# Kernel tuning notes

Hardware: AMD Instinct MI355X
Metric: run time of the kernel (lower is better)

The kernel has to match this reference:

```python
import jax, jax.numpy as jnp
import numpy as np

B, L, D, H = 16, 1024, 128, 256


def setup_inputs() -> dict:
    key = jax.random.key(0)
    ks = jax.random.split(key, 32)
    inp = {
        "x": jax.random.normal(ks[0], (B, L, D), jnp.float32),
        "y": jax.random.normal(ks[1], (B, L, D), jnp.float32),
        "z": jax.random.normal(ks[2], (B, L, D), jnp.float32),
        "len_x": jax.random.randint(ks[3], (B,), L // 2, L + 1, dtype=jnp.int32),
        "len_y": jax.random.randint(ks[4], (B,), L // 2, L + 1, dtype=jnp.int32),
        "len_z": jax.random.randint(ks[5], (B,), L // 2, L + 1, dtype=jnp.int32),
    }
    s1 = (2.0 / (D + H)) ** 0.5  # xavier-normal for first layer
    s2 = (2.0 / (H + D)) ** 0.5
    i = 6
    for name in ("W1", "B1", "W2", "B2"):
        inp[f"{name}_l1_w"] = jax.random.normal(ks[i + 0], (D, H), jnp.float32) * s1
        inp[f"{name}_l1_b"] = jnp.zeros((H,), jnp.float32)
        inp[f"{name}_l2_w"] = jax.random.normal(ks[i + 1], (H, D), jnp.float32) * s2
        inp[f"{name}_l2_b"] = jnp.zeros((D,), jnp.float32)
        i += 2
    return inp


def _mlp(c, w1, b1, w2, b2):
    h = jax.nn.gelu(c @ w1 + b1, approximate=False)  # torch nn.GELU = exact erf form
    return h @ w2 + b2


def _batched_ragged_dft(xc, lengths, inverse):
    # Per-sample DFT over the first lengths[i] timesteps; rows/cols >= l are zero.
    _, Ls, _ = xc.shape
    t = jnp.arange(Ls, dtype=jnp.int32)
    kt = t[:, None] * t[None, :]                      # [L,L] integer k*t
    l = lengths[:, None, None]                        # [B,1,1]
    ktm = kt[None, :, :] % l                          # exact phase reduction mod l
    sign = 1.0 if inverse else -1.0
    phase = sign * 2.0 * jnp.pi * ktm.astype(jnp.float32) / l.astype(jnp.float32)
    mask = (t[None, :, None] < l) & (t[None, None, :] < l)
    E = jnp.where(mask, jnp.exp(1j * phase).astype(jnp.complex64), 0.0)
    if inverse:
        E = E / l.astype(jnp.complex64)
    return jnp.einsum("bkt,btd->bkd", E, xc)


def _complex_relu(f):
    # torch: where(|z|>0, |z|*exp(i*angle(z)), 0)
    mag = jnp.abs(f)
    safe = jnp.where(mag > 0, f, jnp.asarray(1.0 + 0.0j, jnp.complex64))
    act = jnp.abs(safe) * jnp.exp(1j * jnp.angle(safe))
    return jnp.where(mag > 0, act.astype(jnp.complex64), 0.0)


def reference(x, y, z, len_x, len_y, len_z,
              W1_l1_w, W1_l1_b, W1_l2_w, W1_l2_b,
              B1_l1_w, B1_l1_b, B1_l2_w, B1_l2_b,
              W2_l1_w, W2_l1_b, W2_l2_w, W2_l2_b,
              B2_l1_w, B2_l1_b, B2_l2_w, B2_l2_b):
    x_freq = _batched_ragged_dft(x.astype(jnp.complex64), len_x, inverse=False)
    c1 = jnp.sum(y, axis=1) / len_y[:, None].astype(jnp.float32)
    c2 = jnp.sum(z, axis=1) / len_z[:, None].astype(jnp.float32)
    W1 = _mlp(c1, W1_l1_w, W1_l1_b, W1_l2_w, W1_l2_b).astype(jnp.complex64)
    b1 = _mlp(c1, B1_l1_w, B1_l1_b, B1_l2_w, B1_l2_b).astype(jnp.complex64)
    W2 = _mlp(c2, W2_l1_w, W2_l1_b, W2_l2_w, W2_l2_b).astype(jnp.complex64)
    b2 = _mlp(c2, B2_l1_w, B2_l1_b, B2_l2_w, B2_l2_b).astype(jnp.complex64)
    filtered = x_freq * (1.0 + (W1 + W2)[:, None, :] / 2.0) + (b1 + b2)[:, None, :] / 2.0
    activated = _complex_relu(filtered)
    x_recon = _batched_ragged_dft(activated, len_x, inverse=True)
    return x_recon.real
```

## Files before the change

kernel.cpp:

```cpp
#include <hip/hip_runtime.h>
#include <math.h>

constexpr int NB = 16;
constexpr int SL = 1024;
constexpr int ND = 128;
constexpr int NH = 256;
constexpr int NSTILE = 18;
constexpr int NKTILE = 17;
constexpr int EPAD = 584;

constexpr size_t PLANE_S = (size_t)NB * 8 * NSTILE * 1024;
constexpr size_t PLANE_K = (size_t)NB * 8 * NKTILE * 1024;
constexpr size_t CS_OFF = 0;
constexpr size_t DD_OFF = PLANE_S;
constexpr size_t FR_OFF = 2 * PLANE_S;
constexpr size_t FI_OFF = 2 * PLANE_S + PLANE_K;
constexpr size_t F32B      = PLANE_S + PLANE_K;
constexpr size_t P_OFF     = F32B;
constexpr size_t SCALE_OFF = P_OFF + 2 * 16 * 16 * 128;
constexpr size_t BIAS_OFF  = SCALE_OFF + NB * ND;

typedef float          f32x4 __attribute__((ext_vector_type(4)));
typedef unsigned int   u32x4 __attribute__((ext_vector_type(4)));
typedef unsigned short u16x8 __attribute__((ext_vector_type(8)));

__device__ __forceinline__ unsigned short f2bf(float f) {
    unsigned u = __float_as_uint(f);
    return (unsigned short)((u + 0x7FFFu + ((u >> 16) & 1u)) >> 16);
}
__device__ __forceinline__ float hw_sin(float rev) {
    float r; asm("v_sin_f32 %0, %1" : "=v"(r) : "v"(rev)); return r;
}
__device__ __forceinline__ float hw_cos(float rev) {
    float r; asm("v_cos_f32 %0, %1" : "=v"(r) : "v"(rev)); return r;
}
__device__ __forceinline__ void mfma16(f32x4& acc, u32x4 a, u32x4 b) {
    asm("v_mfma_f32_16x16x32_bf16 %0, %1, %2, %0" : "+v"(acc) : "v"(a), "v"(b));
}
__device__ __forceinline__ float4 f4add(float4 a, float4 b) {
    return make_float4(a.x + b.x, a.y + b.y, a.z + b.z, a.w + b.w);
}

__global__ __launch_bounds__(256) void k_front(const float* __restrict__ x,
                                               const float* __restrict__ y,
                                               const float* __restrict__ z,
                                               const int* __restrict__ len_x,
                                               float* __restrict__ wsf,
                                               unsigned short* __restrict__ wsb,
                                               float* __restrict__ out) {
    const int blk = blockIdx.x;
    const int tid = threadIdx.x;
    __shared__ float4 red4[256];

    if (blk < 512) {
        const int ch  = blk & 15;
        const int b   = (blk >> 4) & 15;
        const int src = blk >> 8;
        const float* base = (src == 0 ? y : z) + ((size_t)b * SL + ch * 64) * ND;
        const int dg = tid & 31;
        const int tq = tid >> 5;
        float4 s = make_float4(0.f, 0.f, 0.f, 0.f);
#pragma unroll
        for (int j = 0; j < 8; ++j)
            s = f4add(s, *(const float4*)&base[(size_t)(tq + 8 * j) * ND + dg * 4]);
        red4[tid] = s;
        __syncthreads();
        if (tq < 4) red4[tid] = f4add(red4[tid], red4[tid + 128]);
        __syncthreads();
        if (tq < 2) red4[tid] = f4add(red4[tid], red4[tid + 64]);
        __syncthreads();
        if (tq == 0) {
            const float4 r = f4add(red4[dg], red4[dg + 32]);
            *(float4*)&wsf[P_OFF + ((size_t)((src * NB + b) * 16 + ch)) * ND + dg * 4] = r;
        }
        return;
    }

    if (blk < 800) {
        const int pb = blk - 512;
        const int bx = pb % NSTILE;
        const int b  = pb / NSTILE;
        const int l = len_x[b];
        const int NS = (l >> 1) + 1;
        const int d = tid & 127;
        const int slot = tid >> 7;
        const int dblk = d >> 4, dw = d & 15;
#pragma unroll
        for (int it = 0; it < 2; ++it) {
            const int sb = (bx * 4 + slot * 2 + it) * 8;
            u16x8 cb, db;
#pragma unroll
            for (int j = 0; j < 8; ++j) {
                const int s = sb + j;
                float c = 0.f, dd = 0.f;
                if (s < NS) {
                    const float a = x[((size_t)b * SL + s) * ND + d];
                    float p = 0.f;
                    if (s > 0 && 2 * s != l) p = x[((size_t)b * SL + (l - s)) * ND + d];
                    c = a + p; dd = a - p;
                }
                cb[j] = f2bf(c); db[j] = f2bf(dd);
            }
            const int sg = (sb >> 3) & 3;
            const size_t ro = ((size_t)((b * 8 + dblk) * NSTILE) + bx) * 1024 + sg * 128 + dw * 8;
            *(u16x8*)&wsb[CS_OFF + ro] = cb;
            *(u16x8*)&wsb[DD_OFF + ro] = db;
            if (sb + 7 >= NS && sb < NKTILE * 32) {
                const u16x8 zz = {0, 0, 0, 0, 0, 0, 0, 0};
                const size_t ko = ((size_t)((b * 8 + dblk) * NKTILE) + (sb >> 5)) * 1024 + sg * 128 + dw * 8;
                *(u16x8*)&wsb[FR_OFF + ko] = zz;
                *(u16x8*)&wsb[FI_OFF + ko] = zz;
            }
        }
        return;
    }

    {
        const int zb = blk - 800;
        const int b = zb >> 3;
        const int seg = zb & 7;
        const int l = len_x[b];
        const int row = 512 + seg * 64 + (tid >> 2);
        if (row >= l) {
            const int c16 = (tid & 3) * 32;
            float* p = &out[((size_t)b * SL + row) * ND + c16];
            const float4 zz = make_float4(0.f, 0.f, 0.f, 0.f);
#pragma unroll
            for (int q = 0; q < 8; ++q)
                *(float4*)&p[q * 4] = zz;
        }
        return;
    }
}

__global__ __launch_bounds__(512) void k_fwd_mlp(
    const int* __restrict__ len_x,
    const int* __restrict__ len_y, const int* __restrict__ len_z,
    float* __restrict__ wsf, unsigned short* __restrict__ wsb,
    const float* __restrict__ W1w1, const float* __restrict__ W1b1,
    const float* __restrict__ W1w2, const float* __restrict__ W1b2,
    const float* __restrict__ B1w1, const float* __restrict__ B1b1,
    const float* __restrict__ B1w2, const float* __restrict__ B1b2,
    const float* __restrict__ W2w1, const float* __restrict__ W2b1,
    const float* __restrict__ W2w2, const float* __restrict__ W2b2,
    const float* __restrict__ B2w1, const float* __restrict__ B2b1,
    const float* __restrict__ B2w2, const float* __restrict__ B2b2) {
    const int tid = threadIdx.x;

    if (blockIdx.x >= 528) {
        const int mb = blockIdx.x - 528;
        const int pair = mb & 1;
        const int b    = mb >> 1;

        const float* w1a = pair ? B1w1 : W1w1;  const float* b1a = pair ? B1b1 : W1b1;
        const float* w2a = pair ? B1w2 : W1w2;  const float* b2a = pair ? B1b2 : W1b2;
        const float* w1b = pair ? B2w1 : W2w1;  const float* b1b = pair ? B2b1 : W2b1;
        const float* w2b = pair ? B2w2 : W2w2;  const float* b2b = pair ? B2b2 : W2b2;

        __shared__ float c1s[ND], c2s[ND];
        __shared__ float h0[NH], h1[NH];
        __shared__ float oa[ND], ob[ND];

        if (tid < ND) {
            float s = 0.f;
            for (int ch = 0; ch < 16; ++ch)
                s += wsf[P_OFF + ((size_t)((0 * NB + b) * 16 + ch)) * ND + tid];
            c1s[tid] = s / (float)len_y[b];
        } else if (tid < 256) {
            const int d = tid - ND;
            float s = 0.f;
            for (int ch = 0; ch < 16; ++ch)
                s += wsf[P_OFF + ((size_t)((1 * NB + b) * 16 + ch)) * ND + d];
            c2s[d] = s / (float)len_z[b];
        }
        __syncthreads();

        if (tid < 256) {
            const int j = tid;
            float s0 = b1a[j], s1 = b1b[j];
            for (int i = 0; i < ND; ++i) {
                s0 = fmaf(c1s[i], w1a[i * NH + j], s0);
                s1 = fmaf(c2s[i], w1b[i * NH + j], s1);
            }
            h0[j] = 0.5f * s0 * (1.f + erff(s0 * 0.7071067811865475f));
            h1[j] = 0.5f * s1 * (1.f + erff(s1 * 0.7071067811865475f));
        }
        __syncthreads();

        if (tid < 256) {
            const bool second = tid >= ND;
            const int d = second ? tid - ND : tid;
            const float* w = second ? w2b : w2a;
            const float* hh = second ? h1 : h0;
            float s = second ? b2b[d] : b2a[d];
            for (int j = 0; j < NH; ++j)
                s = fmaf(hh[j], w[j * ND + d], s);
            if (second) ob[d] = s; else oa[d] = s;
        }
        __syncthreads();

        if (tid < ND) {
            if (pair == 0)
                wsf[SCALE_OFF + b * ND + tid] = 1.f + 0.5f * (oa[tid] + ob[tid]);
            else
                wsf[BIAS_OFF  + b * ND + tid] = 0.5f * (oa[tid] + ob[tid]);
        }
        return;
    }

    const int bid = blockIdx.x;
    const int b7 = bid & 7;
    const int q  = bid >> 3;
    const int b  = (q / 33) * 8 + b7;
    const int kbase = (q % 33) * 16;

    const int l = len_x[b];
    const int NS = (l >> 1) + 1;
    if (kbase >= NS) return;
    const float invl = 1.f / (float)l;
    const float fl = (float)l;

    __shared__ __align__(16) unsigned short Ec[16][EPAD];
    __shared__ __align__(16) unsigned short Es[16][EPAD];

    const int lane = tid & 63;
    const int wave8 = tid >> 6;
    const int shalf = wave8 >> 2;
    const int w4    = wave8 & 3;
    const int lrow = lane & 15, lkg = lane >> 4;

    if (tid < 256) {
        const int row = tid >> 4;
        const int colbase = (tid & 15) * 36;
        const int kk = kbase + row;
#pragma unroll 6
        for (int j = 0; j < 36; j += 2) {
            unsigned cw = 0, sw = 0;
#pragma unroll
            for (int h = 0; h < 2; ++h) {
                const int sg = colbase + j + h;
                float cv = 0.f, sv = 0.f;
                if (sg < NS) {
                    const float ks = (float)(kk * sg);
                    float idxf = fmaf(-fl, floorf(ks * invl), ks);
                    idxf = (idxf < 0.f) ? idxf + fl : idxf;
                    const float rev = idxf * invl;
                    cv = hw_cos(rev);
                    sv = -hw_sin(rev);
                }
                cw |= (unsigned)f2bf(cv) << (16 * h);
                sw |= (unsigned)f2bf(sv) << (16 * h);
            }
            *(unsigned*)&Ec[row][colbase + j] = cw;
            *(unsigned*)&Es[row][colbase + j] = sw;
        }
    }
    __syncthreads();

    f32x4 accR[2], accI[2];
#pragma unroll
    for (int t = 0; t < 2; ++t) { accR[t] = 0.f; accI[t] = 0.f; }

    const size_t tb0 = ((size_t)((b * 8 + 2 * w4 + 0) * NSTILE)) * 1024 + lane * 8;
    const size_t tb1 = ((size_t)((b * 8 + 2 * w4 + 1) * NSTILE)) * 1024 + lane * 8;

    const int ntile = (NS + 31) >> 5;
    const int mid = ntile >> 1;
    const int st0 = shalf ? mid : 0;
    const int st1 = shalf ? ntile : mid;

    for (int stile = st0; stile < st1; ++stile) {
        const int s0 = stile * 32;
        const u32x4 eC = *(const u32x4*)&Ec[lrow][s0 + lkg * 8];
        const u32x4 eS = *(const u32x4*)&Es[lrow][s0 + lkg * 8];
        const u32x4 aC0 = *(const u32x4*)&wsb[CS_OFF + tb0 + (size_t)stile * 1024];
        const u32x4 aD0 = *(const u32x4*)&wsb[DD_OFF + tb0 + (size_t)stile * 1024];
        const u32x4 aC1 = *(const u32x4*)&wsb[CS_OFF + tb1 + (size_t)stile * 1024];
        const u32x4 aD1 = *(const u32x4*)&wsb[DD_OFF + tb1 + (size_t)stile * 1024];
        mfma16(accR[0], aC0, eC);
        mfma16(accI[0], aD0, eS);
        mfma16(accR[1], aC1, eC);
        mfma16(accI[1], aD1, eS);
    }

    float* PR = (float*)((char*)&Ec[0][0] + 4096);
    float* PI = (float*)((char*)&Es[0][0] + 4096);

    __syncthreads();
    if (shalf == 1) {
#pragma unroll
        for (int t = 0; t < 2; ++t)
#pragma unroll
            for (int r = 0; r < 4; ++r) {
                const int drow = w4 * 32 + t * 16 + lkg * 4 + r;
                PR[drow * 16 + lrow] = accR[t][r];
                PI[drow * 16 + lrow] = accI[t][r];
            }
    }
    __syncthreads();

    unsigned short (*FRst)[16] = (unsigned short(*)[16])&Ec[0][0];
    unsigned short (*FIst)[16] = (unsigned short(*)[16])&Es[0][0];

    if (shalf == 0) {
        const int kcol = kbase + lrow;
        const float w = ((kcol == 0 || 2 * kcol == l) ? 1.f : 2.f) * invl;
#pragma unroll
        for (int t = 0; t < 2; ++t) {
#pragma unroll
            for (int r = 0; r < 4; ++r) {
                const int drow = w4 * 32 + t * 16 + lkg * 4 + r;
                const float vR = accR[t][r] + PR[drow * 16 + lrow];
                const float vI = accI[t][r] + PI[drow * 16 + lrow];
                FRst[drow][lrow] = f2bf(w * vR);
                FIst[drow][lrow] = f2bf(w * vI);
            }
        }
    }
    __syncthreads();

    if (tid < 256) {
        const int dblk = tid >> 5;
        const int kgi  = (tid >> 4) & 1;
        const int dw   = tid & 15;
        const int ktile = kbase >> 5;
        const int kg0 = (kbase & 16) ? 2 : 0;
        const size_t go = ((size_t)((b * 8 + dblk) * NKTILE) + ktile) * 1024
                        + (kg0 + kgi) * 128 + dw * 8;
        const int d = dblk * 16 + dw;
        if (kbase + 15 < NS) {
            *(u16x8*)&wsb[FR_OFF + go] = *(u16x8*)&FRst[d][kgi * 8];
            *(u16x8*)&wsb[FI_OFF + go] = *(u16x8*)&FIst[d][kgi * 8];
        } else {
            u16x8 fr, fi;
#pragma unroll
            for (int e = 0; e < 8; ++e) {
                const int kc = kbase + kgi * 8 + e;
                fr[e] = (kc < NS) ? FRst[d][kgi * 8 + e] : (unsigned short)0;
                fi[e] = (kc < NS) ? FIst[d][kgi * 8 + e] : (unsigned short)0;
            }
            *(u16x8*)&wsb[FR_OFF + go] = fr;
            *(u16x8*)&wsb[FI_OFF + go] = fi;
        }
    }
}

__global__ __launch_bounds__(512) void k_inv(const int* __restrict__ len_x,
                                             const float* __restrict__ wsf,
                                             const unsigned short* __restrict__ wsb,
                                             float* __restrict__ out) {
    const int bid = blockIdx.x;
    const int b7 = bid & 7;
    const int q  = bid >> 3;
    const int b  = (q / 33) * 8 + b7;
    const int tbase = (q % 33) * 16;

    const int l = len_x[b];
    const int NS = (l >> 1) + 1;
    if (tbase >= NS) return;
    const float invl = 1.f / (float)l;
    const float fl = (float)l;

    __shared__ __align__(16) unsigned short E2c[16][EPAD];
    __shared__ __align__(16) unsigned short E2s[16][EPAD];

    const int tid = threadIdx.x;
    const int lane = tid & 63;
    const int wave8 = tid >> 6;
    const int shalf = wave8 >> 2;
    const int w4    = wave8 & 3;
    const int lrow = lane & 15, lkg = lane >> 4;

    if (tid < 256) {
        const int row = tid >> 4;
        const int colbase = (tid & 15) * 36;
        const int tt = tbase + row;
#pragma unroll 6
        for (int j = 0; j < 36; j += 2) {
            unsigned cw = 0, sw = 0;
#pragma unroll
            for (int h = 0; h < 2; ++h) {
                const int kg = colbase + j + h;
                float cv = 0.f, sv = 0.f;
                if (kg < NS) {
                    const float tk = (float)(tt * kg);
                    float idxf = fmaf(-fl, floorf(tk * invl), tk);
                    idxf = (idxf < 0.f) ? idxf + fl : idxf;
                    const float rev = idxf * invl;
                    cv = hw_cos(rev);
                    sv = hw_sin(rev);
                }
                cw |= (unsigned)f2bf(cv) << (16 * h);
                sw |= (unsigned)f2bf(sv) << (16 * h);
            }
            *(unsigned*)&E2c[row][colbase + j] = cw;
            *(unsigned*)&E2s[row][colbase + j] = sw;
        }
    }
    __syncthreads();

    const int dc0 = w4 * 32 + lrow;
    const int dc1 = w4 * 32 + 16 + lrow;
    const float sc0 = wsf[SCALE_OFF + b * ND + dc0];
    const float sc1 = wsf[SCALE_OFF + b * ND + dc1];
    const float bi0 = wsf[BIAS_OFF + b * ND + dc0];
    const float bi1 = wsf[BIAS_OFF + b * ND + dc1];

    f32x4 accA[2], accB[2];
#pragma unroll
    for (int t = 0; t < 2; ++t) { accA[t] = 0.f; accB[t] = 0.f; }

    const size_t tb0 = ((size_t)((b * 8 + 2 * w4 + 0) * NKTILE)) * 1024 + lane * 8;
    const size_t tb1 = ((size_t)((b * 8 + 2 * w4 + 1) * NKTILE)) * 1024 + lane * 8;

    const int ntile = (NS + 31) >> 5;
    const int mid = ntile >> 1;
    const int kt0 = shalf ? mid : 0;
    const int kt1 = shalf ? ntile : mid;

    for (int ktile = kt0; ktile < kt1; ++ktile) {
        const int k0 = ktile * 32;
        const u32x4 aC = *(const u32x4*)&E2c[lrow][k0 + lkg * 8];
        const u32x4 aS = *(const u32x4*)&E2s[lrow][k0 + lkg * 8];
        const u32x4 bR0 = *(const u32x4*)&wsb[FR_OFF + tb0 + (size_t)ktile * 1024];
        const u32x4 bI0 = *(const u32x4*)&wsb[FI_OFF + tb0 + (size_t)ktile * 1024];
        const u32x4 bR1 = *(const u32x4*)&wsb[FR_OFF + tb1 + (size_t)ktile * 1024];
        const u32x4 bI1 = *(const u32x4*)&wsb[FI_OFF + tb1 + (size_t)ktile * 1024];
        mfma16(accA[0], aC, bR0);
        mfma16(accB[0], aS, bI0);
        mfma16(accA[1], aC, bR1);
        mfma16(accB[1], aS, bI1);
    }

    float* PA = (float*)((char*)&E2c[0][0] + 8192);
    float* PB = (float*)((char*)&E2s[0][0] + 8192);

    __syncthreads();
    if (shalf == 1) {
#pragma unroll
        for (int t = 0; t < 2; ++t)
#pragma unroll
            for (int r = 0; r < 4; ++r) {
                const int dcol = w4 * 32 + t * 16 + lrow;
                PA[dcol * 16 + lkg * 4 + r] = accA[t][r];
                PB[dcol * 16 + lkg * 4 + r] = accB[t][r];
            }
    }
    __syncthreads();

    float (*O1)[ND] = (float(*)[ND])&E2c[0][0];
    float (*O2)[ND] = (float(*)[ND])&E2s[0][0];

    if (shalf == 0) {
#pragma unroll
        for (int t = 0; t < 2; ++t) {
            const int dcol = (t == 0) ? dc0 : dc1;
            const float sc = (t == 0) ? sc0 : sc1;
            const float bi = (t == 0) ? bi0 : bi1;
#pragma unroll
            for (int r = 0; r < 4; ++r) {
                const int ro = lkg * 4 + r;
                const float vA = accA[t][r] + PA[dcol * 16 + ro];
                const float vB = accB[t][r] + PB[dcol * 16 + ro];
                float va = (vA - vB) * sc;
                if (tbase + ro == 0) va += bi;
                O1[ro][dcol] = va;
                O2[ro][dcol] = (vA + vB) * sc;
            }
        }
    }
    __syncthreads();

    if (tid < 256) {
        const int r8 = tid >> 4;
        const int c8 = (tid & 15) * 8;
        const int trow = tbase + r8;
        if (trow < NS) {
            float* p = &out[((size_t)b * SL + trow) * ND + c8];
            *(float4*)p = *(float4*)&O1[r8][c8];
            *(float4*)(p + 4) = *(float4*)&O1[r8][c8 + 4];
            if (trow > 0 && 2 * trow != l) {
                float* q2 = &out[((size_t)b * SL + (l - trow)) * ND + c8];
                *(float4*)q2 = *(float4*)&O2[r8][c8];
                *(float4*)(q2 + 4) = *(float4*)&O2[r8][c8 + 4];
            }
        }
    }
}

extern "C" void kernel_launch(void* const* d_in, const int* in_sizes, int n_in,
                              void* d_out, int out_size, void* d_ws, size_t ws_size,
                              hipStream_t stream) {
    const float* x = (const float*)d_in[0];
    const float* y = (const float*)d_in[1];
    const float* z = (const float*)d_in[2];
    const int* len_x = (const int*)d_in[3];
    const int* len_y = (const int*)d_in[4];
    const int* len_z = (const int*)d_in[5];
    float* wsf = (float*)d_ws;
    unsigned short* wsb = (unsigned short*)d_ws;
    float* out = (float*)d_out;

    k_front<<<928, 256, 0, stream>>>(x, y, z, len_x, wsf, wsb, out);

    k_fwd_mlp<<<560, 512, 0, stream>>>(len_x, len_y, len_z, wsf, wsb,
        (const float*)d_in[6],  (const float*)d_in[7],  (const float*)d_in[8],  (const float*)d_in[9],
        (const float*)d_in[10], (const float*)d_in[11], (const float*)d_in[12], (const float*)d_in[13],
        (const float*)d_in[14], (const float*)d_in[15], (const float*)d_in[16], (const float*)d_in[17],
        (const float*)d_in[18], (const float*)d_in[19], (const float*)d_in[20], (const float*)d_in[21]);

    k_inv<<<528, 512, 0, stream>>>(len_x, wsf, wsb, out);
}
```

Measured before the change: 46.66 us.

## Process two 16-row frequency/time tiles per block to reuse loaded operands

Each block of the forward and inverse DFT kernels now covers 32 output rows instead of 16. It builds two twiddle tiles in shared memory using all 512 threads and issues twice the MFMAs per loaded global operand tile. This halves redundant global reads of the workspace planes and halves the block count. In exchange it doubles shared memory and accumulator registers, reduces parallelism, and makes blocks past NS skip less often.

```diff
diff --git a/kernel.cpp b/kernel.cpp
--- a/kernel.cpp
+++ b/kernel.cpp
@@ -147,8 +147,8 @@
     const float* __restrict__ B2w2, const float* __restrict__ B2b2) {
     const int tid = threadIdx.x;
 
-    if (blockIdx.x >= 528) {
-        const int mb = blockIdx.x - 528;
+    if (blockIdx.x >= 272) {
+        const int mb = blockIdx.x - 272;
         const int pair = mb & 1;
         const int b    = mb >> 1;
 
@@ -211,8 +211,8 @@
     const int bid = blockIdx.x;
     const int b7 = bid & 7;
     const int q  = bid >> 3;
-    const int b  = (q / 33) * 8 + b7;
-    const int kbase = (q % 33) * 16;
+    const int b  = (q / 17) * 8 + b7;
+    const int kbase = (q % 17) * 32;
 
     const int l = len_x[b];
     const int NS = (l >> 1) + 1;
@@ -220,8 +220,8 @@
     const float invl = 1.f / (float)l;
     const float fl = (float)l;
 
-    __shared__ __align__(16) unsigned short Ec[16][EPAD];
-    __shared__ __align__(16) unsigned short Es[16][EPAD];
+    __shared__ __align__(16) unsigned short Ec[2][16][EPAD];
+    __shared__ __align__(16) unsigned short Es[2][16][EPAD];
 
     const int lane = tid & 63;
     const int wave8 = tid >> 6;
@@ -229,10 +229,12 @@
     const int w4    = wave8 & 3;
     const int lrow = lane & 15, lkg = lane >> 4;
 
-    if (tid < 256) {
-        const int row = tid >> 4;
-        const int colbase = (tid & 15) * 36;
-        const int kk = kbase + row;
+    {
+        const int pp = tid >> 8;
+        const int t2 = tid & 255;
+        const int row = t2 >> 4;
+        const int colbase = (t2 & 15) * 36;
+        const int kk = kbase + pp * 16 + row;
 #pragma unroll 6
         for (int j = 0; j < 36; j += 2) {
             unsigned cw = 0, sw = 0;
@@ -251,15 +253,17 @@
                 cw |= (unsigned)f2bf(cv) << (16 * h);
                 sw |= (unsigned)f2bf(sv) << (16 * h);
             }
-            *(unsigned*)&Ec[row][colbase + j] = cw;
-            *(unsigned*)&Es[row][colbase + j] = sw;
+            *(unsigned*)&Ec[pp][row][colbase + j] = cw;
+            *(unsigned*)&Es[pp][row][colbase + j] = sw;
         }
     }
     __syncthreads();
 
-    f32x4 accR[2], accI[2];
-#pragma unroll
-    for (int t = 0; t < 2; ++t) { accR[t] = 0.f; accI[t] = 0.f; }
+    f32x4 accR[2][2], accI[2][2];
+#pragma unroll
+    for (int t = 0; t < 2; ++t)
+#pragma unroll
+        for (int p = 0; p < 2; ++p) { accR[t][p] = 0.f; accI[t][p] = 0.f; }
 
     const size_t tb0 = ((size_t)((b * 8 + 2 * w4 + 0) * NSTILE)) * 1024 + lane * 8;
     const size_t tb1 = ((size_t)((b * 8 + 2 * w4 + 1) * NSTILE)) * 1024 + lane * 8;
@@ -271,76 +275,89 @@
 
     for (int stile = st0; stile < st1; ++stile) {
         const int s0 = stile * 32;
-        const u32x4 eC = *(const u32x4*)&Ec[lrow][s0 + lkg * 8];
-        const u32x4 eS = *(const u32x4*)&Es[lrow][s0 + lkg * 8];
+        const u32x4 eC0 = *(const u32x4*)&Ec[0][lrow][s0 + lkg * 8];
+        const u32x4 eS0 = *(const u32x4*)&Es[0][lrow][s0 + lkg * 8];
+        const u32x4 eC1 = *(const u32x4*)&Ec[1][lrow][s0 + lkg * 8];
+        const u32x4 eS1 = *(const u32x4*)&Es[1][lrow][s0 + lkg * 8];
         const u32x4 aC0 = *(const u32x4*)&wsb[CS_OFF + tb0 + (size_t)stile * 1024];
         const u32x4 aD0 = *(const u32x4*)&wsb[DD_OFF + tb0 + (size_t)stile * 1024];
         const u32x4 aC1 = *(const u32x4*)&wsb[CS_OFF + tb1 + (size_t)stile * 1024];
         const u32x4 aD1 = *(const u32x4*)&wsb[DD_OFF + tb1 + (size_t)stile * 1024];
-        mfma16(accR[0], aC0, eC);
-        mfma16(accI[0], aD0, eS);
-        mfma16(accR[1], aC1, eC);
-        mfma16(accI[1], aD1, eS);
-    }
-
-    float* PR = (float*)((char*)&Ec[0][0] + 4096);
-    float* PI = (float*)((char*)&Es[0][0] + 4096);
+        mfma16(accR[0][0], aC0, eC0);
+        mfma16(accI[0][0], aD0, eS0);
+        mfma16(accR[1][0], aC1, eC0);
+        mfma16(accI[1][0], aD1, eS0);
+        mfma16(accR[0][1], aC0, eC1);
+        mfma16(accI[0][1], aD0, eS1);
+        mfma16(accR[1][1], aC1, eC1);
+        mfma16(accI[1][1], aD1, eS1);
+    }
+
+    float* PR = (float*)((char*)&Ec[0][0][0] + 4096);
+    float* PI = (float*)((char*)&Es[0][0][0] + 4096);
 
     __syncthreads();
     if (shalf == 1) {
 #pragma unroll
         for (int t = 0; t < 2; ++t)
 #pragma unroll
-            for (int r = 0; r < 4; ++r) {
-                const int drow = w4 * 32 + t * 16 + lkg * 4 + r;
-                PR[drow * 16 + lrow] = accR[t][r];
-                PI[drow * 16 + lrow] = accI[t][r];
-            }
+            for (int p = 0; p < 2; ++p)
+#pragma unroll
+                for (int r = 0; r < 4; ++r) {
+                    const int drow = w4 * 32 + t * 16 + lkg * 4 + r;
+                    PR[(p * 128 + drow) * 16 + lrow] = accR[t][p][r];
+                    PI[(p * 128 + drow) * 16 + lrow] = accI[t][p][r];
+                }
     }
     __syncthreads();
 
-    unsigned short (*FRst)[16] = (unsigned short(*)[16])&Ec[0][0];
-    unsigned short (*FIst)[16] = (unsigned short(*)[16])&Es[0][0];
-
-    if (shalf == 0) {
-        const int kcol = kbase + lrow;
-        const float w = ((kcol == 0 || 2 * kcol == l) ? 1.f : 2.f) * invl;
-#pragma unroll
-        for (int t = 0; t < 2; ++t) {
-#pragma unroll
-            for (int r = 0; r < 4; ++r) {
-                const int drow = w4 * 32 + t * 16 + lkg * 4 + r;
-                const float vR = accR[t][r] + PR[drow * 16 + lrow];
-                const float vI = accI[t][r] + PI[drow * 16 + lrow];
-                FRst[drow][lrow] = f2bf(w * vR);
-                FIst[drow][lrow] = f2bf(w * vI);
-            }
-        }
-    }
-    __syncthreads();
-
-    if (tid < 256) {
-        const int dblk = tid >> 5;
-        const int kgi  = (tid >> 4) & 1;
-        const int dw   = tid & 15;
-        const int ktile = kbase >> 5;
-        const int kg0 = (kbase & 16) ? 2 : 0;
-        const size_t go = ((size_t)((b * 8 + dblk) * NKTILE) + ktile) * 1024
-                        + (kg0 + kgi) * 128 + dw * 8;
-        const int d = dblk * 16 + dw;
-        if (kbase + 15 < NS) {
-            *(u16x8*)&wsb[FR_OFF + go] = *(u16x8*)&FRst[d][kgi * 8];
-            *(u16x8*)&wsb[FI_OFF + go] = *(u16x8*)&FIst[d][kgi * 8];
-        } else {
-            u16x8 fr, fi;
-#pragma unroll
-            for (int e = 0; e < 8; ++e) {
-                const int kc = kbase + kgi * 8 + e;
-                fr[e] = (kc < NS) ? FRst[d][kgi * 8 + e] : (unsigned short)0;
-                fi[e] = (kc < NS) ? FIst[d][kgi * 8 + e] : (unsigned short)0;
-            }
-            *(u16x8*)&wsb[FR_OFF + go] = fr;
-            *(u16x8*)&wsb[FI_OFF + go] = fi;
+    unsigned short (*FRst)[16] = (unsigned short(*)[16])&Ec[0][0][0];
+    unsigned short (*FIst)[16] = (unsigned short(*)[16])&Es[0][0][0];
+
+#pragma unroll
+    for (int p = 0; p < 2; ++p) {
+        const int kb2 = kbase + p * 16;
+        if (p) __syncthreads();
+        if (shalf == 0) {
+            const int kcol = kb2 + lrow;
+            const float w = ((kcol == 0 || 2 * kcol == l) ? 1.f : 2.f) * invl;
+#pragma unroll
+            for (int t = 0; t < 2; ++t) {
+#pragma unroll
+                for (int r = 0; r < 4; ++r) {
+                    const int drow = w4 * 32 + t * 16 + lkg * 4 + r;
+                    const float vR = accR[t][p][r] + PR[(p * 128 + drow) * 16 + lrow];
+                    const float vI = accI[t][p][r] + PI[(p * 128 + drow) * 16 + lrow];
+                    FRst[drow][lrow] = f2bf(w * vR);
+                    FIst[drow][lrow] = f2bf(w * vI);
+                }
+            }
+        }
+        __syncthreads();
+
+        if (tid < 256) {
+            const int dblk = tid >> 5;
+            const int kgi  = (tid >> 4) & 1;
+            const int dw   = tid & 15;
+            const int ktile = kb2 >> 5;
+            const int kg0 = (kb2 & 16) ? 2 : 0;
+            const size_t go = ((size_t)((b * 8 + dblk) * NKTILE) + ktile) * 1024
+                            + (kg0 + kgi) * 128 + dw * 8;
+            const int d = dblk * 16 + dw;
+            if (kb2 + 15 < NS) {
+                *(u16x8*)&wsb[FR_OFF + go] = *(u16x8*)&FRst[d][kgi * 8];
+                *(u16x8*)&wsb[FI_OFF + go] = *(u16x8*)&FIst[d][kgi * 8];
+            } else {
+                u16x8 fr, fi;
+#pragma unroll
+                for (int e = 0; e < 8; ++e) {
+                    const int kc = kb2 + kgi * 8 + e;
+                    fr[e] = (kc < NS) ? FRst[d][kgi * 8 + e] : (unsigned short)0;
+                    fi[e] = (kc < NS) ? FIst[d][kgi * 8 + e] : (unsigned short)0;
+                }
+                *(u16x8*)&wsb[FR_OFF + go] = fr;
+                *(u16x8*)&wsb[FI_OFF + go] = fi;
+            }
         }
     }
 }
@@ -352,8 +369,8 @@
     const int bid = blockIdx.x;
     const int b7 = bid & 7;
     const int q  = bid >> 3;
-    const int b  = (q / 33) * 8 + b7;
-    const int tbase = (q % 33) * 16;
+    const int b  = (q / 17) * 8 + b7;
+    const int tbase = (q % 17) * 32;
 
     const int l = len_x[b];
     const int NS = (l >> 1) + 1;
@@ -361,8 +378,8 @@
     const float invl = 1.f / (float)l;
     const float fl = (float)l;
 
-    __shared__ __align__(16) unsigned short E2c[16][EPAD];
-    __shared__ __align__(16) unsigned short E2s[16][EPAD];
+    __shared__ __align__(16) unsigned short E2c[2][16][EPAD];
+    __shared__ __align__(16) unsigned short E2s[2][16][EPAD];
 
     const int tid = threadIdx.x;
     const int lane = tid & 63;
@@ -371,10 +388,12 @@
     const int w4    = wave8 & 3;
     const int lrow = lane & 15, lkg = lane >> 4;
 
-    if (tid < 256) {
-        const int row = tid >> 4;
-        const int colbase = (tid & 15) * 36;
-        const int tt = tbase + row;
+    {
+        const int pp = tid >> 8;
+        const int t2 = tid & 255;
+        const int row = t2 >> 4;
+        const int colbase = (t2 & 15) * 36;
+        const int tt = tbase + pp * 16 + row;
 #pragma unroll 6
         for (int j = 0; j < 36; j += 2) {
             unsigned cw = 0, sw = 0;
@@ -393,8 +412,8 @@
                 cw |= (unsigned)f2bf(cv) << (16 * h);
                 sw |= (unsigned)f2bf(sv) << (16 * h);
             }
-            *(unsigned*)&E2c[row][colbase + j] = cw;
-            *(unsigned*)&E2s[row][colbase + j] = sw;
+            *(unsigned*)&E2c[pp][row][colbase + j] = cw;
+            *(unsigned*)&E2s[pp][row][colbase + j] = sw;
         }
     }
     __syncthreads();
@@ -406,9 +425,11 @@
     const float bi0 = wsf[BIAS_OFF + b * ND + dc0];
     const float bi1 = wsf[BIAS_OFF + b * ND + dc1];
 
-    f32x4 accA[2], accB[2];
-#pragma unroll
-    for (int t = 0; t < 2; ++t) { accA[t] = 0.f; accB[t] = 0.f; }
+    f32x4 accA[2][2], accB[2][2];
+#pragma unroll
+    for (int t = 0; t < 2; ++t)
+#pragma unroll
+        for (int p = 0; p < 2; ++p) { accA[t][p] = 0.f; accB[t][p] = 0.f; }
 
     const size_t tb0 = ((size_t)((b * 8 + 2 * w4 + 0) * NKTILE)) * 1024 + lane * 8;
     const size_t tb1 = ((size_t)((b * 8 + 2 * w4 + 1) * NKTILE)) * 1024 + lane * 8;
@@ -420,69 +441,82 @@
 
     for (int ktile = kt0; ktile < kt1; ++ktile) {
         const int k0 = ktile * 32;
-        const u32x4 aC = *(const u32x4*)&E2c[lrow][k0 + lkg * 8];
-        const u32x4 aS = *(const u32x4*)&E2s[lrow][k0 + lkg * 8];
+        const u32x4 aC0 = *(const u32x4*)&E2c[0][lrow][k0 + lkg * 8];
+        const u32x4 aS0 = *(const u32x4*)&E2s[0][lrow][k0 + lkg * 8];
+        const u32x4 aC1 = *(const u32x4*)&E2c[1][lrow][k0 + lkg * 8];
+        const u32x4 aS1 = *(const u32x4*)&E2s[1][lrow][k0 + lkg * 8];
         const u32x4 bR0 = *(const u32x4*)&wsb[FR_OFF + tb0 + (size_t)ktile * 1024];
         const u32x4 bI0 = *(const u32x4*)&wsb[FI_OFF + tb0 + (size_t)ktile * 1024];
         const u32x4 bR1 = *(const u32x4*)&wsb[FR_OFF + tb1 + (size_t)ktile * 1024];
         const u32x4 bI1 = *(const u32x4*)&wsb[FI_OFF + tb1 + (size_t)ktile * 1024];
-        mfma16(accA[0], aC, bR0);
-        mfma16(accB[0], aS, bI0);
-        mfma16(accA[1], aC, bR1);
-        mfma16(accB[1], aS, bI1);
-    }
-
-    float* PA = (float*)((char*)&E2c[0][0] + 8192);
-    float* PB = (float*)((char*)&E2s[0][0] + 8192);
+        mfma16(accA[0][0], aC0, bR0);
+        mfma16(accB[0][0], aS0, bI0);
+        mfma16(accA[1][0], aC0, bR1);
+        mfma16(accB[1][0], aS0, bI1);
+        mfma16(accA[0][1], aC1, bR0);
+        mfma16(accB[0][1], aS1, bI0);
+        mfma16(accA[1][1], aC1, bR1);
+        mfma16(accB[1][1], aS1, bI1);
+    }
+
+    float* PA = (float*)((char*)&E2c[0][0][0] + 8192);
+    float* PB = (float*)((char*)&E2s[0][0][0] + 8192);
 
     __syncthreads();
     if (shalf == 1) {
 #pragma unroll
         for (int t = 0; t < 2; ++t)
 #pragma unroll
-            for (int r = 0; r < 4; ++r) {
-                const int dcol = w4 * 32 + t * 16 + lrow;
-                PA[dcol * 16 + lkg * 4 + r] = accA[t][r];
-                PB[dcol * 16 + lkg * 4 + r] = accB[t][r];
-            }
+            for (int p = 0; p < 2; ++p)
+#pragma unroll
+                for (int r = 0; r < 4; ++r) {
+                    const int dcol = w4 * 32 + t * 16 + lrow;
+                    PA[(p * 128 + dcol) * 16 + lkg * 4 + r] = accA[t][p][r];
+                    PB[(p * 128 + dcol) * 16 + lkg * 4 + r] = accB[t][p][r];
+                }
     }
     __syncthreads();
 
-    float (*O1)[ND] = (float(*)[ND])&E2c[0][0];
-    float (*O2)[ND] = (float(*)[ND])&E2s[0][0];
-
-    if (shalf == 0) {
-#pragma unroll
-        for (int t = 0; t < 2; ++t) {
-            const int dcol = (t == 0) ? dc0 : dc1;
-            const float sc = (t == 0) ? sc0 : sc1;
-            const float bi = (t == 0) ? bi0 : bi1;
-#pragma unroll
-            for (int r = 0; r < 4; ++r) {
-                const int ro = lkg * 4 + r;
-                const float vA = accA[t][r] + PA[dcol * 16 + ro];
-                const float vB = accB[t][r] + PB[dcol * 16 + ro];
-                float va = (vA - vB) * sc;
-                if (tbase + ro == 0) va += bi;
-                O1[ro][dcol] = va;
-                O2[ro][dcol] = (vA + vB) * sc;
-            }
-        }
-    }
-    __syncthreads();
-
-    if (tid < 256) {
-        const int r8 = tid >> 4;
-        const int c8 = (tid & 15) * 8;
-        const int trow = tbase + r8;
-        if (trow < NS) {
-            float* p = &out[((size_t)b * SL + trow) * ND + c8];
-            *(float4*)p = *(float4*)&O1[r8][c8];
-            *(float4*)(p + 4) = *(float4*)&O1[r8][c8 + 4];
-            if (trow > 0 && 2 * trow != l) {
-                float* q2 = &out[((size_t)b * SL + (l - trow)) * ND + c8];
-                *(float4*)q2 = *(float4*)&O2[r8][c8];
-                *(float4*)(q2 + 4) = *(float4*)&O2[r8][c8 + 4];
+    float (*O1)[ND] = (float(*)[ND])&E2c[0][0][0];
+    float (*O2)[ND] = (float(*)[ND])&E2s[0][0][0];
+
+#pragma unroll
+    for (int p = 0; p < 2; ++p) {
+        const int tb2 = tbase + p * 16;
+        if (p) __syncthreads();
+        if (shalf == 0) {
+#pragma unroll
+            for (int t = 0; t < 2; ++t) {
+                const int dcol = (t == 0) ? dc0 : dc1;
+                const float sc = (t == 0) ? sc0 : sc1;
+                const float bi = (t == 0) ? bi0 : bi1;
+#pragma unroll
+                for (int r = 0; r < 4; ++r) {
+                    const int ro = lkg * 4 + r;
+                    const float vA = accA[t][p][r] + PA[(p * 128 + dcol) * 16 + ro];
+                    const float vB = accB[t][p][r] + PB[(p * 128 + dcol) * 16 + ro];
+                    float va = (vA - vB) * sc;
+                    if (tb2 + ro == 0) va += bi;
+                    O1[ro][dcol] = va;
+                    O2[ro][dcol] = (vA + vB) * sc;
+                }
+            }
+        }
+        __syncthreads();
+
+        if (tid < 256) {
+            const int r8 = tid >> 4;
+            const int c8 = (tid & 15) * 8;
+            const int trow = tb2 + r8;
+            if (trow < NS) {
+                float* pp = &out[((size_t)b * SL + trow) * ND + c8];
+                *(float4*)pp = *(float4*)&O1[r8][c8];
+                *(float4*)(pp + 4) = *(float4*)&O1[r8][c8 + 4];
+                if (trow > 0 && 2 * trow != l) {
+                    float* q2 = &out[((size_t)b * SL + (l - trow)) * ND + c8];
+                    *(float4*)q2 = *(float4*)&O2[r8][c8];
+                    *(float4*)(q2 + 4) = *(float4*)&O2[r8][c8 + 4];
+                }
             }
         }
     }
@@ -503,11 +537,11 @@
 
     k_front<<<928, 256, 0, stream>>>(x, y, z, len_x, wsf, wsb, out);
 
-    k_fwd_mlp<<<560, 512, 0, stream>>>(len_x, len_y, len_z, wsf, wsb,
+    k_fwd_mlp<<<304, 512, 0, stream>>>(len_x, len_y, len_z, wsf, wsb,
         (const float*)d_in[6],  (const float*)d_in[7],  (const float*)d_in[8],  (const float*)d_in[9],
         (const float*)d_in[10], (const float*)d_in[11], (const float*)d_in[12], (const float*)d_in[13],
         (const float*)d_in[14], (const float*)d_in[15], (const float*)d_in[16], (const float*)d_in[17],
         (const float*)d_in[18], (const float*)d_in[19], (const float*)d_in[20], (const float*)d_in[21]);
 
-    k_inv<<<528, 512, 0, stream>>>(len_x, wsf, wsb, out);
-}
+    k_inv<<<272, 512, 0, stream>>>(len_x, wsf, wsb, out);
+}
```

Result: faster. 44.68 us (-4.3%).
